# Kernel tuning notes

Measured on AMD Instinct MI355X. Metric: run time of the kernel, lower is better.

The kernel has to match this reference:

```python
import jax, jax.numpy as jnp
import numpy as np

D_MODEL = 1024
N_HEADS = 16
HEAD_DIM = D_MODEL // N_HEADS


def setup_inputs() -> dict:
    key = jax.random.key(0)
    ks = jax.random.split(key, 12)
    B, S = 1, 4096
    s = 1.0 / np.sqrt(D_MODEL)
    return {
        "query": jax.random.normal(ks[0], (B, S, D_MODEL), jnp.float32),
        "key": jax.random.normal(ks[1], (B, S, D_MODEL), jnp.float32),
        "value": jax.random.normal(ks[2], (B, S, D_MODEL), jnp.float32),
        "attention_mask": jnp.ones((B, S), jnp.int32),
        "Wq": jax.random.normal(ks[3], (D_MODEL, D_MODEL), jnp.float32) * s,
        "bq": jax.random.normal(ks[4], (D_MODEL,), jnp.float32) * s,
        "Wk": jax.random.normal(ks[5], (D_MODEL, D_MODEL), jnp.float32) * s,
        "bk": jax.random.normal(ks[6], (D_MODEL,), jnp.float32) * s,
        "Wv": jax.random.normal(ks[7], (D_MODEL, D_MODEL), jnp.float32) * s,
        "bv": jax.random.normal(ks[8], (D_MODEL,), jnp.float32) * s,
        "Wo": jax.random.normal(ks[9], (D_MODEL, D_MODEL), jnp.float32) * s,
        "bo": jax.random.normal(ks[10], (D_MODEL,), jnp.float32) * s,
    }


def reference(query, key, value, attention_mask, Wq, bq, Wk, bk, Wv, bv, Wo, bo):
    B = query.shape[0]

    def split_heads(x):  # [B,S,D] -> [B,H,S,Dh]
        return x.reshape(B, -1, N_HEADS, HEAD_DIM).transpose(0, 2, 1, 3)

    q = split_heads(query @ Wq + bq)
    k = split_heads(key @ Wk + bk)
    v = split_heads(value @ Wv + bv)

    scores = jnp.einsum("bhqd,bhkd->bhqk", q, k) / np.sqrt(HEAD_DIM)
    # 2D mask [B, Skv] -> [B,1,1,Skv]; 0 positions filled with -1e9
    mask = attention_mask[:, None, None, :]
    scores = jnp.where(mask == 0, jnp.float32(-1e9), scores)
    weights = jax.nn.softmax(scores, axis=-1)
    out = jnp.einsum("bhqk,bhkd->bhqd", weights, v)
    out = out.transpose(0, 2, 1, 3).reshape(B, -1, D_MODEL)
    return out @ Wo + bo
```

## Files before the change

### kernel.cpp

```cpp
#include <hip/hip_runtime.h>
#include <hip/hip_bf16.h>
#include <cstdint>

typedef __attribute__((ext_vector_type(8))) short short8;
typedef __attribute__((ext_vector_type(4))) float floatx4;
typedef unsigned short u16;

#define D_MODEL 1024
#define S_LEN 4096
#define N_HEADS 16
#define HEAD_DIM 64
#define SCALE_LOG2E 0.18033688f

__device__ __forceinline__ u16 f2bf(float x) {
    union { float f; uint32_t u; } v; v.f = x;
    uint32_t u = v.u;
    u += 0x7fffu + ((u >> 16) & 1u);
    return (u16)(u >> 16);
}

__device__ __forceinline__ void load_lds16(const u16* g, u16* l) {
    __builtin_amdgcn_global_load_lds(
        (const __attribute__((address_space(1))) uint32_t*)g,
        (__attribute__((address_space(3))) uint32_t*)l, 16, 0, 0);
}

struct Conv3 { const float* s[3]; u16* d[3]; };
__global__ __launch_bounds__(256) void convert3(Conv3 a, int n4) {
    const int z = blockIdx.y;
    const float* __restrict__ src = a.s[z];
    u16* __restrict__ dst = a.d[z];
    int i = blockIdx.x * 256 + threadIdx.x;
    if (i >= n4) return;
    float4 v = reinterpret_cast<const float4*>(src)[i];
    ushort4 o;
    o.x = f2bf(v.x); o.y = f2bf(v.y); o.z = f2bf(v.z); o.w = f2bf(v.w);
    reinterpret_cast<ushort4*>(dst)[i] = o;
}

__global__ __launch_bounds__(256) void mask_to_madd(const int* __restrict__ m,
                                                    float* __restrict__ o, int n4) {
    int i = blockIdx.x * 256 + threadIdx.x;
    if (i >= n4) return;
    int4 mv = reinterpret_cast<const int4*>(m)[i];
    float4 f;
    f.x = mv.x == 0 ? -1.0e30f : 0.f;
    f.y = mv.y == 0 ? -1.0e30f : 0.f;
    f.z = mv.z == 0 ? -1.0e30f : 0.f;
    f.w = mv.w == 0 ? -1.0e30f : 0.f;
    reinterpret_cast<float4*>(o)[i] = f;
}

struct Tr4 { const float* s[4]; u16* d[4]; };
__global__ __launch_bounds__(256) void transpose4(Tr4 a, int R, int C) {
    __shared__ u16 tile[32][34];
    const int z = blockIdx.z;
    const float* __restrict__ in = a.s[z];
    u16* __restrict__ out = a.d[z];
    const int tx = threadIdx.x, ty = threadIdx.y;
    const int c0 = blockIdx.x * 32, r0 = blockIdx.y * 32;
    #pragma unroll
    for (int j = 0; j < 32; j += 8)
        tile[ty + j][tx] = f2bf(in[(size_t)(r0 + ty + j) * C + c0 + tx]);
    __syncthreads();
    #pragma unroll
    for (int j = 0; j < 32; j += 8)
        out[(size_t)(c0 + ty + j) * R + r0 + tx] = tile[tx][ty + j];
}

template <typename OutT>
__device__ __forceinline__ void gemm_bt_core(const u16* __restrict__ A, const u16* __restrict__ Bt,
                                             const float* __restrict__ bias, OutT* __restrict__ C,
                                             int M, int N, int K, int bx, int by, int trC) {
    __shared__ u16 As[128 * 64];
    __shared__ u16 Bs[128 * 64];
    const int tid = threadIdx.x;
    const int wave = tid >> 6, lane = tid & 63;
    const int quad = lane >> 4, n16 = lane & 15;
    const int wm = wave >> 1, wn = wave & 1;
    const int m0 = by * 128, n0 = bx * 128;
    const int rl = lane >> 3, cl = lane & 7;

    floatx4 acc[4][4];
    #pragma unroll
    for (int i = 0; i < 4; ++i)
        #pragma unroll
        for (int t = 0; t < 4; ++t) acc[i][t] = (floatx4)0.f;

    for (int kt = 0; kt < K; kt += 64) {
        __syncthreads();
        #pragma unroll
        for (int u = 0; u < 4; ++u) {
            const int r = wave * 32 + u * 8 + rl;
            const int c = cl ^ (rl & 7);
            load_lds16(&A[(size_t)(m0 + r) * K + kt + c * 8], &As[(wave * 32 + u * 8) * 64]);
            load_lds16(&Bt[(size_t)(n0 + r) * K + kt + c * 8], &Bs[(wave * 32 + u * 8) * 64]);
        }
        __syncthreads();
        #pragma unroll
        for (int kk = 0; kk < 2; ++kk) {
            short8 a[4], b[4];
            #pragma unroll
            for (int i = 0; i < 4; ++i) {
                const int row = wm * 64 + i * 16 + n16;
                const int sw = ((kk * 4 + quad) ^ (n16 & 7)) * 8;
                a[i] = *reinterpret_cast<const short8*>(&As[row * 64 + sw]);
            }
            #pragma unroll
            for (int t = 0; t < 4; ++t) {
                const int row = wn * 64 + t * 16 + n16;
                const int sw = ((kk * 4 + quad) ^ (n16 & 7)) * 8;
                b[t] = *reinterpret_cast<const short8*>(&Bs[row * 64 + sw]);
            }
            #pragma unroll
            for (int i = 0; i < 4; ++i)
                #pragma unroll
                for (int t = 0; t < 4; ++t)
                    acc[i][t] = __builtin_amdgcn_mfma_f32_16x16x32_bf16(a[i], b[t], acc[i][t], 0, 0, 0);
        }
    }
    #pragma unroll
    for (int t = 0; t < 4; ++t) {
        const int col = n0 + wn * 64 + t * 16 + n16;
        const float bv = bias[col];
        #pragma unroll
        for (int i = 0; i < 4; ++i) {
            #pragma unroll
            for (int r = 0; r < 4; ++r) {
                const int row = m0 + wm * 64 + i * 16 + quad * 4 + r;
                const float val = acc[i][t][r] + bv;
                const size_t idx = trC ? ((size_t)col * M + row) : ((size_t)row * N + col);
                if constexpr (sizeof(OutT) == 2) C[idx] = f2bf(val);
                else                             C[idx] = val;
            }
        }
    }
}

struct QkvArgs {
    const u16* A[3]; const u16* B[3]; const float* bias[3]; u16* C[3];
};

__global__ __launch_bounds__(256) void gemm_qkv(QkvArgs args, int M, int N, int K) {
    const int z = blockIdx.z;
    gemm_bt_core<u16>(args.A[z], args.B[z], args.bias[z], args.C[z], M, N, K,
                      blockIdx.x, blockIdx.y, z == 2 ? 1 : 0);
}

__global__ __launch_bounds__(256) void gemm_out(const u16* __restrict__ A, const u16* __restrict__ Bt,
                                                const float* __restrict__ bias, float* __restrict__ C,
                                                int M, int N, int K) {
    gemm_bt_core<float>(A, Bt, bias, C, M, N, K, blockIdx.x, blockIdx.y, 0);
}

__global__ __launch_bounds__(256) void flash_attn(const u16* __restrict__ Q, const u16* __restrict__ Kb,
                                                  const u16* __restrict__ Vt,
                                                  const float* __restrict__ madd,
                                                  u16* __restrict__ O) {
    __shared__ u16 Ks[2][64 * 64];
    __shared__ u16 Vs[2][64 * 64];
    __shared__ u16 Ps[4][16 * 64];
    const int tid = threadIdx.x;
    const int wave = tid >> 6, lane = tid & 63;
    const int quad = lane >> 4, n16 = lane & 15;
    const int bid = blockIdx.x;
    const int h = (bid & 7) * 2 + ((bid >> 3) & 1);
    const int qt = bid >> 4;
    const int hd = h * HEAD_DIM;
    const int q0 = qt * 64 + wave * 16;

    const int rl = lane >> 3, cl = lane & 7;
    const int swz = n16 & 7;

    short8 b_q[2];
    #pragma unroll
    for (int kk = 0; kk < 2; ++kk)
        b_q[kk] = *reinterpret_cast<const short8*>(
            &Q[(size_t)(q0 + n16) * D_MODEL + hd + kk * 32 + quad * 8]);

    float l_i = 0.f;
    floatx4 o_acc[4];
    #pragma unroll
    for (int t = 0; t < 4; ++t) o_acc[t] = (floatx4)0.f;

    #pragma unroll
    for (int u = 0; u < 2; ++u) {
        const int r = wave * 16 + u * 8 + rl;
        const int c = cl ^ (rl & 7);
        load_lds16(&Kb[(size_t)r * D_MODEL + hd + c * 8], &Ks[0][(wave * 16 + u * 8) * 64]);
        load_lds16(&Vt[(size_t)(hd + r) * S_LEN + c * 8], &Vs[0][(wave * 16 + u * 8) * 64]);
    }

    #pragma unroll 1
    for (int it2 = 0; it2 < 32; ++it2) {
        #pragma unroll
        for (int half = 0; half < 2; ++half) {
            const int it = it2 * 2 + half;
            const int cur = half;
            const int k0 = it * 64;
            __syncthreads();

            const int kn = ((it + 1) & 63) * 64;
            #pragma unroll
            for (int u = 0; u < 2; ++u) {
                const int r = wave * 16 + u * 8 + rl;
                const int c = cl ^ (rl & 7);
                load_lds16(&Kb[(size_t)(kn + r) * D_MODEL + hd + c * 8],
                           &Ks[cur ^ 1][(wave * 16 + u * 8) * 64]);
                load_lds16(&Vt[(size_t)(hd + r) * S_LEN + kn + c * 8],
                           &Vs[cur ^ 1][(wave * 16 + u * 8) * 64]);
            }

            floatx4 s[4];
            #pragma unroll
            for (int t = 0; t < 4; ++t) {
                s[t] = (floatx4)0.f;
                #pragma unroll
                for (int kk = 0; kk < 2; ++kk) {
                    const int sw = ((kk * 4 + quad) ^ swz) * 8;
                    short8 ak = *reinterpret_cast<const short8*>(&Ks[cur][(t * 16 + n16) * 64 + sw]);
                    s[t] = __builtin_amdgcn_mfma_f32_16x16x32_bf16(ak, b_q[kk], s[t], 0, 0, 0);
                }
            }
            #pragma unroll
            for (int t = 0; t < 4; ++t) {
                const float4 mv = *reinterpret_cast<const float4*>(&madd[k0 + t * 16 + quad * 4]);
                const float p0 = __builtin_amdgcn_exp2f(fmaf(s[t][0], SCALE_LOG2E, mv.x));
                const float p1 = __builtin_amdgcn_exp2f(fmaf(s[t][1], SCALE_LOG2E, mv.y));
                const float p2 = __builtin_amdgcn_exp2f(fmaf(s[t][2], SCALE_LOG2E, mv.z));
                const float p3 = __builtin_amdgcn_exp2f(fmaf(s[t][3], SCALE_LOG2E, mv.w));
                l_i += (p0 + p1) + (p2 + p3);
                union { __hip_bfloat162 h; uint32_t u; } pa, pb;
                pa.h = __float22bfloat162_rn(make_float2(p0, p1));
                pb.h = __float22bfloat162_rn(make_float2(p2, p3));
                uint2 w; w.x = pa.u; w.y = pb.u;
                const int cw = t * 2 + (quad >> 1);
                *reinterpret_cast<uint2*>(
                    &Ps[wave][n16 * 64 + ((cw ^ swz) * 8 + (quad & 1) * 4)]) = w;
            }
            asm volatile("s_waitcnt lgkmcnt(0)" ::: "memory");
            short8 ap[2];
            #pragma unroll
            for (int kkv = 0; kkv < 2; ++kkv)
                ap[kkv] = *reinterpret_cast<const short8*>(
                    &Ps[wave][n16 * 64 + ((kkv * 4 + quad) ^ swz) * 8]);
            asm volatile("" ::: "memory");
            #pragma unroll
            for (int t = 0; t < 4; ++t) {
                #pragma unroll
                for (int kkv = 0; kkv < 2; ++kkv) {
                    const int sw = ((kkv * 4 + quad) ^ swz) * 8;
                    short8 bv = *reinterpret_cast<const short8*>(&Vs[cur][(t * 16 + n16) * 64 + sw]);
                    o_acc[t] = __builtin_amdgcn_mfma_f32_16x16x32_bf16(ap[kkv], bv, o_acc[t], 0, 0, 0);
                }
            }
        }
    }
    float lt = l_i;
    lt += __shfl_xor(lt, 16);
    lt += __shfl_xor(lt, 32);
    const float inv_l = 1.f / lt;
    float lir[4];
    #pragma unroll
    for (int r = 0; r < 4; ++r) lir[r] = __shfl(inv_l, quad * 4 + r);
    #pragma unroll
    for (int t = 0; t < 4; ++t)
        #pragma unroll
        for (int r = 0; r < 4; ++r)
            O[(size_t)(q0 + quad * 4 + r) * D_MODEL + hd + t * 16 + n16] =
                f2bf(o_acc[t][r] * lir[r]);
}

extern "C" void kernel_launch(void* const* d_in, const int* in_sizes, int n_in,
                              void* d_out, int out_size, void* d_ws, size_t ws_size,
                              hipStream_t stream) {
    const float* query = (const float*)d_in[0];
    const float* key   = (const float*)d_in[1];
    const float* value = (const float*)d_in[2];
    const int*   mask  = (const int*)d_in[3];
    const float* Wq = (const float*)d_in[4];
    const float* bq = (const float*)d_in[5];
    const float* Wk = (const float*)d_in[6];
    const float* bk = (const float*)d_in[7];
    const float* Wv = (const float*)d_in[8];
    const float* bv = (const float*)d_in[9];
    const float* Wo = (const float*)d_in[10];
    const float* bo = (const float*)d_in[11];
    float* out = (float*)d_out;

    char* ws = (char*)d_ws;
    const size_t SZ_SD = (size_t)S_LEN * D_MODEL * 2;
    const size_t SZ_W  = (size_t)D_MODEL * D_MODEL * 2;
    u16* qb  = (u16*)(ws);
    u16* kb  = (u16*)(ws + SZ_SD);
    u16* vb  = (u16*)(ws + 2 * SZ_SD);
    u16* Wqt = (u16*)(ws + 3 * SZ_SD);
    u16* Wkt = (u16*)(ws + 3 * SZ_SD + SZ_W);
    u16* Wvt = (u16*)(ws + 3 * SZ_SD + 2 * SZ_W);
    u16* Wot = (u16*)(ws + 3 * SZ_SD + 3 * SZ_W);
    u16* Qp  = (u16*)(ws + 3 * SZ_SD + 4 * SZ_W);
    u16* Kp  = (u16*)(ws + 4 * SZ_SD + 4 * SZ_W);
    u16* Vpt = (u16*)(ws + 5 * SZ_SD + 4 * SZ_W);
    float* maddf = (float*)(ws + 6 * SZ_SD + 4 * SZ_W);
    u16* Oa  = kb;

    const int n4 = S_LEN * D_MODEL / 4;
    Conv3 cv;
    cv.s[0] = query; cv.s[1] = key; cv.s[2] = value;
    cv.d[0] = qb;    cv.d[1] = kb;  cv.d[2] = vb;
    convert3<<<dim3(n4 / 256, 3), 256, 0, stream>>>(cv, n4);

    mask_to_madd<<<dim3(4), 256, 0, stream>>>(mask, maddf, S_LEN / 4);

    Tr4 tr;
    tr.s[0] = Wq; tr.s[1] = Wk; tr.s[2] = Wv; tr.s[3] = Wo;
    tr.d[0] = Wqt; tr.d[1] = Wkt; tr.d[2] = Wvt; tr.d[3] = Wot;
    transpose4<<<dim3(32, 32, 4), dim3(32, 8), 0, stream>>>(tr, D_MODEL, D_MODEL);

    QkvArgs qa;
    qa.A[0] = qb;  qa.A[1] = kb;  qa.A[2] = vb;
    qa.B[0] = Wqt; qa.B[1] = Wkt; qa.B[2] = Wvt;
    qa.bias[0] = bq; qa.bias[1] = bk; qa.bias[2] = bv;
    qa.C[0] = Qp; qa.C[1] = Kp; qa.C[2] = Vpt;
    gemm_qkv<<<dim3(8, 32, 3), 256, 0, stream>>>(qa, S_LEN, D_MODEL, D_MODEL);

    flash_attn<<<dim3(1024), 256, 0, stream>>>(Qp, Kp, Vpt, maddf, Oa);

    gemm_out<<<dim3(8, 32), 256, 0, stream>>>(Oa, Wot, bo, out, S_LEN, D_MODEL, D_MODEL);
}
```

Baseline: 319.9 us.

## Restructure flash attention with 8-wave blocks, triple buffering, and folded softmax scale

```diff
diff --git a/kernel.cpp b/kernel.cpp
--- a/kernel.cpp
+++ b/kernel.cpp
@@ -38,30 +38,28 @@
     reinterpret_cast<ushort4*>(dst)[i] = o;
 }
 
-__global__ __launch_bounds__(256) void mask_to_madd(const int* __restrict__ m,
-                                                    float* __restrict__ o, int n4) {
-    int i = blockIdx.x * 256 + threadIdx.x;
-    if (i >= n4) return;
-    int4 mv = reinterpret_cast<const int4*>(m)[i];
-    float4 f;
-    f.x = mv.x == 0 ? -1.0e30f : 0.f;
-    f.y = mv.y == 0 ? -1.0e30f : 0.f;
-    f.z = mv.z == 0 ? -1.0e30f : 0.f;
-    f.w = mv.w == 0 ? -1.0e30f : 0.f;
-    reinterpret_cast<float4*>(o)[i] = f;
-}
-
-struct Tr4 { const float* s[4]; u16* d[4]; };
+__global__ __launch_bounds__(64) void mask_prep(const int* __restrict__ m,
+                                                float* __restrict__ madd,
+                                                int* __restrict__ clean) {
+    const int t = blockIdx.x, lane = threadIdx.x;
+    const int v = m[t * 64 + lane];
+    madd[t * 64 + lane] = (v == 0) ? -1.0e30f : 0.f;
+    const unsigned long long bal = __ballot(v != 0);
+    if (lane == 0) clean[t] = (bal == ~0ull) ? 1 : 0;
+}
+
+struct Tr4 { const float* s[4]; u16* d[4]; float scale[4]; };
 __global__ __launch_bounds__(256) void transpose4(Tr4 a, int R, int C) {
     __shared__ u16 tile[32][34];
     const int z = blockIdx.z;
     const float* __restrict__ in = a.s[z];
     u16* __restrict__ out = a.d[z];
+    const float sc = a.scale[z];
     const int tx = threadIdx.x, ty = threadIdx.y;
     const int c0 = blockIdx.x * 32, r0 = blockIdx.y * 32;
     #pragma unroll
     for (int j = 0; j < 32; j += 8)
-        tile[ty + j][tx] = f2bf(in[(size_t)(r0 + ty + j) * C + c0 + tx]);
+        tile[ty + j][tx] = f2bf(in[(size_t)(r0 + ty + j) * C + c0 + tx] * sc);
     __syncthreads();
     #pragma unroll
     for (int j = 0; j < 32; j += 8)
@@ -71,7 +69,8 @@
 template <typename OutT>
 __device__ __forceinline__ void gemm_bt_core(const u16* __restrict__ A, const u16* __restrict__ Bt,
                                              const float* __restrict__ bias, OutT* __restrict__ C,
-                                             int M, int N, int K, int bx, int by, int trC) {
+                                             int M, int N, int K, int bx, int by, int trC,
+                                             float bscale) {
     __shared__ u16 As[128 * 64];
     __shared__ u16 Bs[128 * 64];
     const int tid = threadIdx.x;
@@ -102,15 +101,13 @@
             short8 a[4], b[4];
             #pragma unroll
             for (int i = 0; i < 4; ++i) {
-                const int row = wm * 64 + i * 16 + n16;
                 const int sw = ((kk * 4 + quad) ^ (n16 & 7)) * 8;
-                a[i] = *reinterpret_cast<const short8*>(&As[row * 64 + sw]);
+                a[i] = *reinterpret_cast<const short8*>(&As[(wm * 64 + i * 16 + n16) * 64 + sw]);
             }
             #pragma unroll
             for (int t = 0; t < 4; ++t) {
-                const int row = wn * 64 + t * 16 + n16;
                 const int sw = ((kk * 4 + quad) ^ (n16 & 7)) * 8;
-                b[t] = *reinterpret_cast<const short8*>(&Bs[row * 64 + sw]);
+                b[t] = *reinterpret_cast<const short8*>(&Bs[(wn * 64 + t * 16 + n16) * 64 + sw]);
             }
             #pragma unroll
             for (int i = 0; i < 4; ++i)
@@ -122,13 +119,13 @@
     #pragma unroll
     for (int t = 0; t < 4; ++t) {
         const int col = n0 + wn * 64 + t * 16 + n16;
-        const float bv = bias[col];
+        const float bvs = bias[col] * bscale;
         #pragma unroll
         for (int i = 0; i < 4; ++i) {
             #pragma unroll
             for (int r = 0; r < 4; ++r) {
                 const int row = m0 + wm * 64 + i * 16 + quad * 4 + r;
-                const float val = acc[i][t][r] + bv;
+                const float val = acc[i][t][r] + bvs;
                 const size_t idx = trC ? ((size_t)col * M + row) : ((size_t)row * N + col);
                 if constexpr (sizeof(OutT) == 2) C[idx] = f2bf(val);
                 else                             C[idx] = val;
@@ -138,28 +135,29 @@
 }
 
 struct QkvArgs {
-    const u16* A[3]; const u16* B[3]; const float* bias[3]; u16* C[3];
+    const u16* A[3]; const u16* B[3]; const float* bias[3]; u16* C[3]; float bscale[3];
 };
 
 __global__ __launch_bounds__(256) void gemm_qkv(QkvArgs args, int M, int N, int K) {
     const int z = blockIdx.z;
     gemm_bt_core<u16>(args.A[z], args.B[z], args.bias[z], args.C[z], M, N, K,
-                      blockIdx.x, blockIdx.y, z == 2 ? 1 : 0);
+                      blockIdx.x, blockIdx.y, z == 2 ? 1 : 0, args.bscale[z]);
 }
 
 __global__ __launch_bounds__(256) void gemm_out(const u16* __restrict__ A, const u16* __restrict__ Bt,
                                                 const float* __restrict__ bias, float* __restrict__ C,
                                                 int M, int N, int K) {
-    gemm_bt_core<float>(A, Bt, bias, C, M, N, K, blockIdx.x, blockIdx.y, 0);
-}
-
-__global__ __launch_bounds__(256) void flash_attn(const u16* __restrict__ Q, const u16* __restrict__ Kb,
+    gemm_bt_core<float>(A, Bt, bias, C, M, N, K, blockIdx.x, blockIdx.y, 0, 1.0f);
+}
+
+__global__ __launch_bounds__(512) void flash_attn(const u16* __restrict__ Q, const u16* __restrict__ Kb,
                                                   const u16* __restrict__ Vt,
                                                   const float* __restrict__ madd,
+                                                  const int* __restrict__ clean,
                                                   u16* __restrict__ O) {
-    __shared__ u16 Ks[2][64 * 64];
-    __shared__ u16 Vs[2][64 * 64];
-    __shared__ u16 Ps[4][16 * 64];
+    __shared__ u16 Ks[3 * 64 * 64];
+    __shared__ u16 Vs[3 * 64 * 64];
+    __shared__ u16 Ps[8][16 * 64];
     const int tid = threadIdx.x;
     const int wave = tid >> 6, lane = tid & 63;
     const int quad = lane >> 4, n16 = lane & 15;
@@ -167,10 +165,13 @@
     const int h = (bid & 7) * 2 + ((bid >> 3) & 1);
     const int qt = bid >> 4;
     const int hd = h * HEAD_DIM;
-    const int q0 = qt * 64 + wave * 16;
+    const int q0 = qt * 128 + wave * 16;
 
     const int rl = lane >> 3, cl = lane & 7;
     const int swz = n16 & 7;
+    const int stg_row = wave * 8 + rl;
+    const int stg_c = (cl ^ (rl & 7)) * 8;
+    const int ldst = (wave * 8) * 64;
 
     short8 b_q[2];
     #pragma unroll
@@ -178,58 +179,52 @@
         b_q[kk] = *reinterpret_cast<const short8*>(
             &Q[(size_t)(q0 + n16) * D_MODEL + hd + kk * 32 + quad * 8]);
 
-    float l_i = 0.f;
+    short8 vone;
+    #pragma unroll
+    for (int i = 0; i < 8; ++i) vone[i] = (short)0x3F80;
+
     floatx4 o_acc[4];
+    floatx4 l_acc = (floatx4)0.f;
     #pragma unroll
     for (int t = 0; t < 4; ++t) o_acc[t] = (floatx4)0.f;
 
     #pragma unroll
-    for (int u = 0; u < 2; ++u) {
-        const int r = wave * 16 + u * 8 + rl;
-        const int c = cl ^ (rl & 7);
-        load_lds16(&Kb[(size_t)r * D_MODEL + hd + c * 8], &Ks[0][(wave * 16 + u * 8) * 64]);
-        load_lds16(&Vt[(size_t)(hd + r) * S_LEN + c * 8], &Vs[0][(wave * 16 + u * 8) * 64]);
+    for (int p = 0; p < 2; ++p) {
+        load_lds16(&Kb[(size_t)(p * 64 + stg_row) * D_MODEL + hd + stg_c], &Ks[p * 4096 + ldst]);
+        load_lds16(&Vt[(size_t)(hd + stg_row) * S_LEN + p * 64 + stg_c], &Vs[p * 4096 + ldst]);
     }
 
+    int cur = 0;
     #pragma unroll 1
-    for (int it2 = 0; it2 < 32; ++it2) {
-        #pragma unroll
-        for (int half = 0; half < 2; ++half) {
-            const int it = it2 * 2 + half;
-            const int cur = half;
-            const int k0 = it * 64;
-            __syncthreads();
-
-            const int kn = ((it + 1) & 63) * 64;
-            #pragma unroll
-            for (int u = 0; u < 2; ++u) {
-                const int r = wave * 16 + u * 8 + rl;
-                const int c = cl ^ (rl & 7);
-                load_lds16(&Kb[(size_t)(kn + r) * D_MODEL + hd + c * 8],
-                           &Ks[cur ^ 1][(wave * 16 + u * 8) * 64]);
-                load_lds16(&Vt[(size_t)(hd + r) * S_LEN + kn + c * 8],
-                           &Vs[cur ^ 1][(wave * 16 + u * 8) * 64]);
-            }
-
-            floatx4 s[4];
+    for (int it = 0; it < 64; ++it) {
+        asm volatile("s_waitcnt vmcnt(2)\n\ts_barrier" ::: "memory");
+
+        const int nb = (cur >= 1) ? cur - 1 : 2;
+        const int kn = ((it + 2) & 63) * 64;
+        load_lds16(&Kb[(size_t)(kn + stg_row) * D_MODEL + hd + stg_c], &Ks[nb * 4096 + ldst]);
+        load_lds16(&Vt[(size_t)(hd + stg_row) * S_LEN + kn + stg_c], &Vs[nb * 4096 + ldst]);
+
+        const u16* KsC = &Ks[cur * 4096];
+        const u16* VsC = &Vs[cur * 4096];
+
+        floatx4 s[4];
+        #pragma unroll
+        for (int t = 0; t < 4; ++t) {
+            s[t] = (floatx4)0.f;
+            #pragma unroll
+            for (int kk = 0; kk < 2; ++kk) {
+                const int sw = ((kk * 4 + quad) ^ swz) * 8;
+                short8 ak = *reinterpret_cast<const short8*>(&KsC[(t * 16 + n16) * 64 + sw]);
+                s[t] = __builtin_amdgcn_mfma_f32_16x16x32_bf16(ak, b_q[kk], s[t], 0, 0, 0);
+            }
+        }
+        if (clean[it]) {
             #pragma unroll
             for (int t = 0; t < 4; ++t) {
-                s[t] = (floatx4)0.f;
-                #pragma unroll
-                for (int kk = 0; kk < 2; ++kk) {
-                    const int sw = ((kk * 4 + quad) ^ swz) * 8;
-                    short8 ak = *reinterpret_cast<const short8*>(&Ks[cur][(t * 16 + n16) * 64 + sw]);
-                    s[t] = __builtin_amdgcn_mfma_f32_16x16x32_bf16(ak, b_q[kk], s[t], 0, 0, 0);
-                }
-            }
-            #pragma unroll
-            for (int t = 0; t < 4; ++t) {
-                const float4 mv = *reinterpret_cast<const float4*>(&madd[k0 + t * 16 + quad * 4]);
-                const float p0 = __builtin_amdgcn_exp2f(fmaf(s[t][0], SCALE_LOG2E, mv.x));
-                const float p1 = __builtin_amdgcn_exp2f(fmaf(s[t][1], SCALE_LOG2E, mv.y));
-                const float p2 = __builtin_amdgcn_exp2f(fmaf(s[t][2], SCALE_LOG2E, mv.z));
-                const float p3 = __builtin_amdgcn_exp2f(fmaf(s[t][3], SCALE_LOG2E, mv.w));
-                l_i += (p0 + p1) + (p2 + p3);
+                const float p0 = __builtin_amdgcn_exp2f(s[t][0]);
+                const float p1 = __builtin_amdgcn_exp2f(s[t][1]);
+                const float p2 = __builtin_amdgcn_exp2f(s[t][2]);
+                const float p3 = __builtin_amdgcn_exp2f(s[t][3]);
                 union { __hip_bfloat162 h; uint32_t u; } pa, pb;
                 pa.h = __float22bfloat162_rn(make_float2(p0, p1));
                 pb.h = __float22bfloat162_rn(make_float2(p2, p3));
@@ -238,31 +233,47 @@
                 *reinterpret_cast<uint2*>(
                     &Ps[wave][n16 * 64 + ((cw ^ swz) * 8 + (quad & 1) * 4)]) = w;
             }
-            asm volatile("s_waitcnt lgkmcnt(0)" ::: "memory");
-            short8 ap[2];
-            #pragma unroll
-            for (int kkv = 0; kkv < 2; ++kkv)
-                ap[kkv] = *reinterpret_cast<const short8*>(
-                    &Ps[wave][n16 * 64 + ((kkv * 4 + quad) ^ swz) * 8]);
-            asm volatile("" ::: "memory");
+        } else {
+            const int k0 = it * 64;
             #pragma unroll
             for (int t = 0; t < 4; ++t) {
-                #pragma unroll
-                for (int kkv = 0; kkv < 2; ++kkv) {
-                    const int sw = ((kkv * 4 + quad) ^ swz) * 8;
-                    short8 bv = *reinterpret_cast<const short8*>(&Vs[cur][(t * 16 + n16) * 64 + sw]);
-                    o_acc[t] = __builtin_amdgcn_mfma_f32_16x16x32_bf16(ap[kkv], bv, o_acc[t], 0, 0, 0);
-                }
-            }
-        }
+                const float4 mv = *reinterpret_cast<const float4*>(&madd[k0 + t * 16 + quad * 4]);
+                const float p0 = __builtin_amdgcn_exp2f(s[t][0] + mv.x);
+                const float p1 = __builtin_amdgcn_exp2f(s[t][1] + mv.y);
+                const float p2 = __builtin_amdgcn_exp2f(s[t][2] + mv.z);
+                const float p3 = __builtin_amdgcn_exp2f(s[t][3] + mv.w);
+                union { __hip_bfloat162 h; uint32_t u; } pa, pb;
+                pa.h = __float22bfloat162_rn(make_float2(p0, p1));
+                pb.h = __float22bfloat162_rn(make_float2(p2, p3));
+                uint2 w; w.x = pa.u; w.y = pb.u;
+                const int cw = t * 2 + (quad >> 1);
+                *reinterpret_cast<uint2*>(
+                    &Ps[wave][n16 * 64 + ((cw ^ swz) * 8 + (quad & 1) * 4)]) = w;
+            }
+        }
+        asm volatile("s_waitcnt lgkmcnt(0)" ::: "memory");
+        short8 ap[2];
+        #pragma unroll
+        for (int kkv = 0; kkv < 2; ++kkv)
+            ap[kkv] = *reinterpret_cast<const short8*>(
+                &Ps[wave][n16 * 64 + ((kkv * 4 + quad) ^ swz) * 8]);
+        asm volatile("" ::: "memory");
+        #pragma unroll
+        for (int kkv = 0; kkv < 2; ++kkv) {
+            l_acc = __builtin_amdgcn_mfma_f32_16x16x32_bf16(ap[kkv], vone, l_acc, 0, 0, 0);
+            #pragma unroll
+            for (int t = 0; t < 4; ++t) {
+                const int sw = ((kkv * 4 + quad) ^ swz) * 8;
+                short8 bv = *reinterpret_cast<const short8*>(&VsC[(t * 16 + n16) * 64 + sw]);
+                o_acc[t] = __builtin_amdgcn_mfma_f32_16x16x32_bf16(ap[kkv], bv, o_acc[t], 0, 0, 0);
+            }
+        }
+        cur = (cur >= 2) ? 0 : cur + 1;
     }
-    float lt = l_i;
-    lt += __shfl_xor(lt, 16);
-    lt += __shfl_xor(lt, 32);
-    const float inv_l = 1.f / lt;
+    asm volatile("s_waitcnt vmcnt(0)" ::: "memory");
     float lir[4];
     #pragma unroll
-    for (int r = 0; r < 4; ++r) lir[r] = __shfl(inv_l, quad * 4 + r);
+    for (int r = 0; r < 4; ++r) lir[r] = 1.f / l_acc[r];
     #pragma unroll
     for (int t = 0; t < 4; ++t)
         #pragma unroll
@@ -302,6 +313,7 @@
     u16* Kp  = (u16*)(ws + 4 * SZ_SD + 4 * SZ_W);
     u16* Vpt = (u16*)(ws + 5 * SZ_SD + 4 * SZ_W);
     float* maddf = (float*)(ws + 6 * SZ_SD + 4 * SZ_W);
+    int* cleanf  = (int*)(ws + 6 * SZ_SD + 4 * SZ_W + S_LEN * sizeof(float));
     u16* Oa  = kb;
 
     const int n4 = S_LEN * D_MODEL / 4;
@@ -310,11 +322,12 @@
     cv.d[0] = qb;    cv.d[1] = kb;  cv.d[2] = vb;
     convert3<<<dim3(n4 / 256, 3), 256, 0, stream>>>(cv, n4);
 
-    mask_to_madd<<<dim3(4), 256, 0, stream>>>(mask, maddf, S_LEN / 4);
+    mask_prep<<<dim3(S_LEN / 64), 64, 0, stream>>>(mask, maddf, cleanf);
 
     Tr4 tr;
     tr.s[0] = Wq; tr.s[1] = Wk; tr.s[2] = Wv; tr.s[3] = Wo;
     tr.d[0] = Wqt; tr.d[1] = Wkt; tr.d[2] = Wvt; tr.d[3] = Wot;
+    tr.scale[0] = SCALE_LOG2E; tr.scale[1] = 1.f; tr.scale[2] = 1.f; tr.scale[3] = 1.f;
     transpose4<<<dim3(32, 32, 4), dim3(32, 8), 0, stream>>>(tr, D_MODEL, D_MODEL);
 
     QkvArgs qa;
@@ -322,9 +335,10 @@
     qa.B[0] = Wqt; qa.B[1] = Wkt; qa.B[2] = Wvt;
     qa.bias[0] = bq; qa.bias[1] = bk; qa.bias[2] = bv;
     qa.C[0] = Qp; qa.C[1] = Kp; qa.C[2] = Vpt;
+    qa.bscale[0] = SCALE_LOG2E; qa.bscale[1] = 1.f; qa.bscale[2] = 1.f;
     gemm_qkv<<<dim3(8, 32, 3), 256, 0, stream>>>(qa, S_LEN, D_MODEL, D_MODEL);
 
-    flash_attn<<<dim3(1024), 256, 0, stream>>>(Qp, Kp, Vpt, maddf, Oa);
+    flash_attn<<<dim3(512), 512, 0, stream>>>(Qp, Kp, Vpt, maddf, cleanf, Oa);
 
     gemm_out<<<dim3(8, 32), 256, 0, stream>>>(Oa, Wot, bo, out, S_LEN, D_MODEL, D_MODEL);
 }
```

New measurement: 286.6 us. -10.4%, faster.
